# Optimization experiments

Measured on AMD Instinct MI355X. Metric: run time of the kernel, lower is better.

Reference implementation:

```python
import jax, jax.numpy as jnp
import numpy as np

BETA = 0.05
KNN = 6
N_SPLITS = 10


def setup_inputs() -> dict:
    key = jax.random.key(0)
    k1, k2, k3 = jax.random.split(key, 3)
    B, C, F = 256, 32768, 2048
    inputs = jax.random.normal(k1, (B, F), dtype=jnp.float32)
    inputs = inputs / jnp.linalg.norm(inputs, axis=1, keepdims=True)  # re-ID features are L2-normalized
    em = jax.random.normal(k2, (C, F), dtype=jnp.float32)
    em = em / jnp.linalg.norm(em, axis=1, keepdims=True)  # memory rows kept unit-norm by EMA update
    targets = jax.random.randint(k3, (B,), 0, C, dtype=jnp.int64)
    return {"inputs": inputs, "em": em, "targets": targets, "epoch": 10}


def reference(inputs, em, targets, epoch):
    B, Fdim = inputs.shape
    C = em.shape[0]
    step = -(-Fdim // N_SPLITS)  # ceil, matches step+=1 logic in torch

    # full similarity against memory bank: [B, C]
    sim = (inputs @ em.T) / BETA

    # per-feature-split similarities: [n_splits, B, C]
    sims = jnp.stack([
        (inputs[:, step * i: min(step * (i + 1), Fdim)]
         @ em[:, step * i: min(step * (i + 1), Fdim)].T) / BETA
        for i in range(N_SPLITS)
    ])

    logp = jax.nn.log_softmax(sim, axis=1)  # [B, C]

    if KNN > 0 and epoch > 4:
        # top-k neighbors per split (descending sort -> first k)
        _, topk = jax.lax.top_k(sims, KNN)  # [n_splits, B, KNN]
        s_idx = jnp.arange(N_SPLITS)[:, None, None]
        b_idx = jnp.arange(B)[None, :, None]
        # scatter uniform weight 1/k at knn indices, then force 1.0 at the true target
        onehot = jnp.zeros((N_SPLITS, B, C), dtype=sim.dtype)
        onehot = onehot.at[s_idx, b_idx, topk].set(1.0 / KNN)
        onehot = onehot.at[jnp.arange(N_SPLITS)[:, None],
                           jnp.arange(B)[None, :],
                           targets[None, :]].set(1.0)
        # mean over splits of mean_b sum_c -(t * log p)
        loss = (-(onehot * logp[None, :, :]).sum(axis=2)).mean(axis=1).mean()
    else:
        loss = -jnp.take_along_axis(logp, targets[:, None], axis=1).mean()
    return loss
```

## Files before the change

kernel.cpp:

```cpp
#include <hip/hip_runtime.h>
#include <stdint.h>


typedef float f32x4 __attribute__((ext_vector_type(4)));
typedef __bf16 bf16x8 __attribute__((ext_vector_type(8)));
typedef unsigned short u16x8 __attribute__((ext_vector_type(8)));

#define NB 256
#define NC 32768
#define NF 2048
#define NSPLIT 10
#define SPLITW 205
#define BN 64
#define NBLK (NC / BN)
#define NKSTEP 64
#define INV_BETA 20.0f
#define UNRL _Pragma("unroll")

__device__ __forceinline__ unsigned short f2bf(float f) {
  uint32_t u = __float_as_uint(f);
  return (unsigned short)((u + 0x7FFFu + ((u >> 16) & 1u)) >> 16);
}
__device__ __forceinline__ bf16x8 asbf(u16x8 v) {
  union { u16x8 u; bf16x8 b; } x; x.u = v; return x.b;
}

#define GLDS16(g, p) __builtin_amdgcn_global_load_lds(                         \
    (const __attribute__((address_space(1))) unsigned int*)(g),                \
    (__attribute__((address_space(3))) unsigned int*)(p), 16, 0, 0)

__global__ __launch_bounds__(256)
void k_zero(float* __restrict__ sumexp, float* __restrict__ out) {
  int t = threadIdx.x;
  if (t < NB) sumexp[t] = 0.f;
  if (t == 0) out[0] = 0.f;
}


#define ISSUE_A(BB, TT) do {                                                   \
  UNRL for (int j_ = 0; j_ < 4; j_++) {                                        \
    const int c_ = w * 4 + j_;                                                 \
    const float* g_ = inp + (size_t)(c_ * 8 + arr) * NF + (TT) * 32 + ag * 4;  \
    GLDS16(g_, &Af[BB][c_ * 256]);                                             \
  }                                                                            \
} while (0)

#define FINALIZE(S) do {                                                       \
  UNRL for (int m_ = 0; m_ < 2; m_++)                                          \
    UNRL for (int n_ = 0; n_ < 4; n_++) accT[m_][n_] += accS[m_][n_];          \
  UNRL for (int m_ = 0; m_ < 2; m_++) {                                        \
    UNRL for (int j_ = 0; j_ < 4; j_++) {                                      \
      uint32_t p_[4];                                                          \
      UNRL for (int n_ = 0; n_ < 4; n_++) {                                    \
        uint32_t u_ = __float_as_uint(accS[m_][n_][j_]);                       \
        u_ ^= (uint32_t)(((int32_t)u_) >> 31) | 0x80000000u;                   \
        p_[n_] = (u_ & 0xFFFFFF80u) | (uint32_t)(n_ * 16 + li);                \
      }                                                                        \
      uint32_t res_[6];                                                        \
      UNRL for (int r_ = 0; r_ < 6; r_++) {                                    \
        uint32_t mx_ = p_[0];                                                  \
        UNRL for (int n_ = 1; n_ < 4; n_++) mx_ = mx_ > p_[n_] ? mx_ : p_[n_]; \
        UNRL for (int d_ = 1; d_ < 16; d_ <<= 1) {                             \
          uint32_t o_ = __shfl_xor(mx_, d_);                                   \
          mx_ = mx_ > o_ ? mx_ : o_;                                           \
        }                                                                      \
        res_[r_] = mx_;                                                        \
        UNRL for (int n_ = 0; n_ < 4; n_++)                                    \
          p_[n_] = (p_[n_] == mx_) ? 0u : p_[n_];                              \
      }                                                                        \
      if (li == 0) {                                                           \
        const int rowg_ = w * 32 + m_ * 16 + lg * 4 + j_;                      \
        uint32_t* dst_ = cand + ((size_t)((S) * NB + rowg_) * NBLK + bx) * 6;  \
        UNRL for (int r_ = 0; r_ < 6; r_++) dst_[r_] = res_[r_];               \
      }                                                                        \
    }                                                                          \
    UNRL for (int n_ = 0; n_ < 4; n_++) accS[m_][n_] = Z4;                     \
  }                                                                            \
} while (0)

#define MFMA_ALL(AF) do {                                                      \
  UNRL for (int m_ = 0; m_ < 2; m_++)                                          \
    UNRL for (int n_ = 0; n_ < 4; n_++)                                        \
      accS[m_][n_] = __builtin_amdgcn_mfma_f32_16x16x32_bf16(                  \
          asbf((AF)[m_]), asbf(bfv_[n_]), accS[m_][n_], 0, 0, 0);              \
} while (0)

#define STEP(TT, CB, NBUF, PRE) do {                                           \
  f32x4 bv_ = {0.f, 0.f, 0.f, 0.f};                                            \
  if (PRE) {                                                                   \
    ISSUE_A(NBUF, (TT) + 1);                                                   \
    bv_ = *(const f32x4*)(em + (size_t)(c0 + br) * NF + ((TT) + 1) * 32 + bg * 4); \
  }                                                                            \
  u16x8 af_[2];                                                                \
  UNRL for (int m_ = 0; m_ < 2; m_++) {                                        \
    const int chunk_ = w * 4 + m_ * 2 + (li >> 3);                             \
    const int rr_ = li & 7;                                                    \
    const float* bp_ = &Af[CB][chunk_ * 256 + rr_ * 32];                       \
    f32x4 x0_ = *(const f32x4*)(bp_ + (((lg << 1)) ^ rr_) * 4);                \
    f32x4 x1_ = *(const f32x4*)(bp_ + (((lg << 1) | 1) ^ rr_) * 4);            \
    af_[m_][0] = f2bf(x0_[0]); af_[m_][1] = f2bf(x0_[1]);                      \
    af_[m_][2] = f2bf(x0_[2]); af_[m_][3] = f2bf(x0_[3]);                      \
    af_[m_][4] = f2bf(x1_[0]); af_[m_][5] = f2bf(x1_[1]);                      \
    af_[m_][6] = f2bf(x1_[2]); af_[m_][7] = f2bf(x1_[3]);                      \
  }                                                                            \
  u16x8 bfv_[4];                                                               \
  UNRL for (int n_ = 0; n_ < 4; n_++) {                                        \
    const int rowp_ = n_ * 16 + li;                                            \
    const int sl_ = lg ^ ((rowp_ >> 1) & 3);                                   \
    bfv_[n_] = *(const u16x8*)&Bh[CB][rowp_ * 32 + sl_ * 8];                   \
  }                                                                            \
  const int k0_ = (TT) * 32;                                                   \
  const int s0_ = k0_ / SPLITW, s1_ = (k0_ + 31) / SPLITW;                     \
  if (s1_ > s0_) {                                                             \
    const int thr_ = s1_ * SPLITW - k0_;                                       \
    u16x8 am_[2];                                                              \
    UNRL for (int m_ = 0; m_ < 2; m_++)                                        \
      UNRL for (int e_ = 0; e_ < 8; e_++)                                      \
        am_[m_][e_] = (lg * 8 + e_) < thr_ ? af_[m_][e_] : (unsigned short)0;  \
    MFMA_ALL(am_);                                                             \
    FINALIZE(s0_);                                                             \
    UNRL for (int m_ = 0; m_ < 2; m_++)                                        \
      UNRL for (int e_ = 0; e_ < 8; e_++)                                      \
        am_[m_][e_] = (lg * 8 + e_) < thr_ ? (unsigned short)0 : af_[m_][e_];  \
    MFMA_ALL(am_);                                                             \
  } else {                                                                     \
    MFMA_ALL(af_);                                                             \
  }                                                                            \
  if (PRE) {                                                                   \
    ushort4 hh_;                                                               \
    hh_.x = f2bf(bv_[0]); hh_.y = f2bf(bv_[1]);                                \
    hh_.z = f2bf(bv_[2]); hh_.w = f2bf(bv_[3]);                                \
    *(ushort4*)&Bh[NBUF][br * 32 + bus * 8 + bh2 * 4] = hh_;                   \
  }                                                                            \
  __syncthreads();                                                             \
} while (0)

__global__ __launch_bounds__(512, 4)
void k_main(const float* __restrict__ inp, const float* __restrict__ em,
            float* __restrict__ sim, uint32_t* __restrict__ cand,
            float* __restrict__ sumexp) {
  __shared__ float Af[2][8192];
  __shared__ unsigned short Bh[2][2048];

  const int t  = threadIdx.x;
  const int l  = t & 63;
  const int w  = t >> 6;
  const int li = l & 15, lg = l >> 4;
  const int bx = blockIdx.x;
  const int c0 = bx * BN;

  const int arr = l >> 3;
  const int ag  = (l & 7) ^ arr;
  const int br  = t >> 3, bg = t & 7;
  const int bus = (bg >> 1) ^ ((br >> 1) & 3);
  const int bh2 = bg & 1;

  const f32x4 Z4 = {0.f, 0.f, 0.f, 0.f};
  f32x4 accT[2][4], accS[2][4];
  UNRL for (int m = 0; m < 2; m++)
    UNRL for (int n = 0; n < 4; n++) { accT[m][n] = Z4; accS[m][n] = Z4; }

  {
    ISSUE_A(0, 0);
    f32x4 bv = *(const f32x4*)(em + (size_t)(c0 + br) * NF + bg * 4);
    ushort4 hh;
    hh.x = f2bf(bv[0]); hh.y = f2bf(bv[1]); hh.z = f2bf(bv[2]); hh.w = f2bf(bv[3]);
    *(ushort4*)&Bh[0][br * 32 + bus * 8 + bh2 * 4] = hh;
    __syncthreads();
  }
  for (int tt2 = 0; tt2 < 31; ++tt2) {
    STEP(2 * tt2, 0, 1, 1);
    STEP(2 * tt2 + 1, 1, 0, 1);
  }
  STEP(62, 0, 1, 1);
  STEP(63, 1, 0, 0);
  FINALIZE(NSPLIT - 1);

  UNRL for (int m = 0; m < 2; m++) {
    UNRL for (int j = 0; j < 4; j++) {
      const int rowg = w * 32 + m * 16 + lg * 4 + j;
      float se = 0.f;
      UNRL for (int n = 0; n < 4; n++) {
        float v = accT[m][n][j] * INV_BETA;
        sim[(size_t)rowg * NC + c0 + n * 16 + li] = v;
        se += __expf(v);
      }
      UNRL for (int d = 1; d < 16; d <<= 1) se += __shfl_xor(se, d);
      if (li == 0) atomicAdd(&sumexp[rowg], se);
    }
  }
}

__device__ __forceinline__ void casd(unsigned long long& a, unsigned long long& b) {
  unsigned long long mx = a > b ? a : b;
  unsigned long long mn = a > b ? b : a;
  a = mx; b = mn;
}

__device__ __forceinline__ void merge8(unsigned long long* a,
                                       const unsigned long long* b) {
  unsigned long long hi[8];
  UNRL for (int i = 0; i < 8; i++) {
    unsigned long long x = a[i], y = b[7 - i];
    hi[i] = x > y ? x : y;
  }
  casd(hi[0], hi[4]); casd(hi[1], hi[5]); casd(hi[2], hi[6]); casd(hi[3], hi[7]);
  casd(hi[0], hi[2]); casd(hi[1], hi[3]); casd(hi[4], hi[6]); casd(hi[5], hi[7]);
  casd(hi[0], hi[1]); casd(hi[2], hi[3]); casd(hi[4], hi[5]); casd(hi[6], hi[7]);
  UNRL for (int i = 0; i < 8; i++) a[i] = hi[i];
}

__global__ __launch_bounds__(64)
void k_m1(const uint32_t* __restrict__ cand,
          unsigned long long* __restrict__ part) {
  const int bx = blockIdx.x;
  const int s = bx >> 11;
  const int b = (bx >> 3) & 255;
  const int g = bx & 7;
  const int l = threadIdx.x;

  const uint32_t* src = cand + ((size_t)(s * NB + b) * NBLK + g * 64) * 6;
  unsigned long long t8[8];
  UNRL for (int i = 0; i < 8; i++) t8[i] = 0ull;

  UNRL for (int i = 0; i < 6; i++) {
    const int idx = l + i * 64;
    const uint32_t e = src[idx];
    const uint32_t colg = (uint32_t)(g * 64 + idx / 6) * 64u + (e & 63u);
    unsigned long long v = ((unsigned long long)(e & 0xFFFFFF80u) << 32)
                         | (unsigned long long)(0xFFFFu ^ colg);
    UNRL for (int k = 0; k < 8; k++) {
      if (v > t8[k]) { unsigned long long tmp = t8[k]; t8[k] = v; v = tmp; }
    }
  }
  UNRL for (int d = 1; d < 64; d <<= 1) {
    unsigned long long o[8];
    UNRL for (int i = 0; i < 8; i++) o[i] = __shfl_xor(t8[i], d);
    merge8(t8, o);
  }
  if (l == 0) {
    unsigned long long* dst = part + ((size_t)(s * NB + b) * 8 + g) * 6;
    UNRL for (int r = 0; r < 6; r++) dst[r] = t8[r];
  }
}

__global__ __launch_bounds__(64)
void k_m2(const unsigned long long* __restrict__ part,
          const float* __restrict__ sim, const float* __restrict__ sumexp,
          const int* __restrict__ tgt, float* __restrict__ out) {
  const int s = blockIdx.x >> 8;
  const int b = blockIdx.x & 255;
  const int l = threadIdx.x;

  unsigned long long t8[8];
  UNRL for (int i = 0; i < 8; i++) t8[i] = 0ull;
  t8[0] = (l < 48) ? part[(size_t)(s * NB + b) * 48 + l] : 0ull;

  UNRL for (int d = 1; d < 64; d <<= 1) {
    unsigned long long o[8];
    UNRL for (int i = 0; i < 8; i++) o[i] = __shfl_xor(t8[i], d);
    merge8(t8, o);
  }
  if (l == 0) {
    const int tg = tgt[b];
    const float lz = logf(sumexp[b]);
    float acc = 0.f; int cnt = 0;
    UNRL for (int r = 0; r < 6; r++) {
      const int col = (int)(((unsigned)(t8[r] & 0xFFFFull)) ^ 0xFFFFu);
      if (col != tg) { acc += sim[(size_t)b * NC + col]; cnt++; }
    }
    const float simt = sim[(size_t)b * NC + tg];
    const float contrib = (simt - lz) + (acc - (float)cnt * lz) * (1.0f / 6.0f);
    atomicAdd(out, -contrib * (1.0f / (NSPLIT * NB)));
  }
}

extern "C" void kernel_launch(void* const* d_in, const int* in_sizes, int n_in,
                              void* d_out, int out_size, void* d_ws, size_t ws_size,
                              hipStream_t stream) {
  const float* inp = (const float*)d_in[0];
  const float* em  = (const float*)d_in[1];
  const int*   tgt = (const int*)d_in[2];
  float* out = (float*)d_out;

  char* ws = (char*)d_ws;
  float* sim = (float*)ws;
  size_t off = (size_t)NB * NC * 4;
  uint32_t* cand = (uint32_t*)(ws + off);
  off += (size_t)NSPLIT * NB * NBLK * 6 * 4;
  unsigned long long* part = (unsigned long long*)(ws + off);
  off += (size_t)NSPLIT * NB * 8 * 6 * 8;
  float* sumexp = (float*)(ws + off);

  k_zero<<<1, 256, 0, stream>>>(sumexp, out);
  k_main<<<NBLK, 512, 0, stream>>>(inp, em, sim, cand, sumexp);
  k_m1<<<NSPLIT * NB * 8, 64, 0, stream>>>(cand, part);
  k_m2<<<NSPLIT * NB, 64, 0, stream>>>(part, sim, sumexp, tgt, out);
}
```

Before: 837.9 us.

## Replace LDS-staged block GEMM with per-wave tiles loading directly from global

Drops the shared-memory double-buffered 512-thread block, which covered all 256 rows against 64 columns. Each 64-thread wave now computes a 32x64 tile, reading bf16 A and fp32 em rows straight from global memory into MFMA fragments. A separate pre-pass converts the input matrix to bf16 once. This removes LDS staging and barriers, but each em tile is now read by 8 row-groups instead of once, which raises global/L2 traffic and relies on cache hits. The loads are uncoalesced row-strided 32-byte accesses.

```diff
diff --git a/kernel.cpp b/kernel.cpp
--- a/kernel.cpp
+++ b/kernel.cpp
@@ -11,23 +11,16 @@
 #define NF 2048
 #define NSPLIT 10
 #define SPLITW 205
-#define BN 64
-#define NBLK (NC / BN)
+#define WM 32
+#define WN 64
+#define NBLK (NC / WN)
 #define NKSTEP 64
 #define INV_BETA 20.0f
 #define UNRL _Pragma("unroll")
 
-__device__ __forceinline__ unsigned short f2bf(float f) {
-  uint32_t u = __float_as_uint(f);
-  return (unsigned short)((u + 0x7FFFu + ((u >> 16) & 1u)) >> 16);
-}
 __device__ __forceinline__ bf16x8 asbf(u16x8 v) {
   union { u16x8 u; bf16x8 b; } x; x.u = v; return x.b;
 }
-
-#define GLDS16(g, p) __builtin_amdgcn_global_load_lds(                         \
-    (const __attribute__((address_space(1))) unsigned int*)(g),                \
-    (__attribute__((address_space(3))) unsigned int*)(p), 16, 0, 0)
 
 __global__ __launch_bounds__(256)
 void k_zero(float* __restrict__ sumexp, float* __restrict__ out) {
@@ -36,14 +29,17 @@
   if (t == 0) out[0] = 0.f;
 }
 
-
-#define ISSUE_A(BB, TT) do {                                                   \
-  UNRL for (int j_ = 0; j_ < 4; j_++) {                                        \
-    const int c_ = w * 4 + j_;                                                 \
-    const float* g_ = inp + (size_t)(c_ * 8 + arr) * NF + (TT) * 32 + ag * 4;  \
-    GLDS16(g_, &Af[BB][c_ * 256]);                                             \
-  }                                                                            \
-} while (0)
+__global__ __launch_bounds__(256)
+void k_cvtA(const float* __restrict__ inp, unsigned short* __restrict__ abf) {
+  const int idx = (blockIdx.x * 256 + threadIdx.x) * 8;
+  f32x4 v0 = *(const f32x4*)(inp + idx);
+  f32x4 v1 = *(const f32x4*)(inp + idx + 4);
+  union { bf16x8 b; u16x8 u; } cv;
+  UNRL for (int e = 0; e < 4; e++) cv.b[e] = (__bf16)v0[e];
+  UNRL for (int e = 0; e < 4; e++) cv.b[4 + e] = (__bf16)v1[e];
+  *(u16x8*)(abf + idx) = cv.u;
+}
+
 
 #define FINALIZE(S) do {                                                       \
   UNRL for (int m_ = 0; m_ < 2; m_++)                                          \
@@ -69,8 +65,8 @@
           p_[n_] = (p_[n_] == mx_) ? 0u : p_[n_];                              \
       }                                                                        \
       if (li == 0) {                                                           \
-        const int rowg_ = w * 32 + m_ * 16 + lg * 4 + j_;                      \
-        uint32_t* dst_ = cand + ((size_t)((S) * NB + rowg_) * NBLK + bx) * 6;  \
+        const int rowg_ = r0 + m_ * 16 + lg * 4 + j_;                          \
+        uint32_t* dst_ = cand + ((size_t)((S) * NB + rowg_) * NBLK + cb) * 6;  \
         UNRL for (int r_ = 0; r_ < 6; r_++) dst_[r_] = res_[r_];               \
       }                                                                        \
     }                                                                          \
@@ -82,103 +78,64 @@
   UNRL for (int m_ = 0; m_ < 2; m_++)                                          \
     UNRL for (int n_ = 0; n_ < 4; n_++)                                        \
       accS[m_][n_] = __builtin_amdgcn_mfma_f32_16x16x32_bf16(                  \
-          asbf((AF)[m_]), asbf(bfv_[n_]), accS[m_][n_], 0, 0, 0);              \
+          asbf((AF)[m_]), bfv_[n_], accS[m_][n_], 0, 0, 0);                    \
 } while (0)
 
-#define STEP(TT, CB, NBUF, PRE) do {                                           \
-  f32x4 bv_ = {0.f, 0.f, 0.f, 0.f};                                            \
-  if (PRE) {                                                                   \
-    ISSUE_A(NBUF, (TT) + 1);                                                   \
-    bv_ = *(const f32x4*)(em + (size_t)(c0 + br) * NF + ((TT) + 1) * 32 + bg * 4); \
-  }                                                                            \
-  u16x8 af_[2];                                                                \
-  UNRL for (int m_ = 0; m_ < 2; m_++) {                                        \
-    const int chunk_ = w * 4 + m_ * 2 + (li >> 3);                             \
-    const int rr_ = li & 7;                                                    \
-    const float* bp_ = &Af[CB][chunk_ * 256 + rr_ * 32];                       \
-    f32x4 x0_ = *(const f32x4*)(bp_ + (((lg << 1)) ^ rr_) * 4);                \
-    f32x4 x1_ = *(const f32x4*)(bp_ + (((lg << 1) | 1) ^ rr_) * 4);            \
-    af_[m_][0] = f2bf(x0_[0]); af_[m_][1] = f2bf(x0_[1]);                      \
-    af_[m_][2] = f2bf(x0_[2]); af_[m_][3] = f2bf(x0_[3]);                      \
-    af_[m_][4] = f2bf(x1_[0]); af_[m_][5] = f2bf(x1_[1]);                      \
-    af_[m_][6] = f2bf(x1_[2]); af_[m_][7] = f2bf(x1_[3]);                      \
-  }                                                                            \
-  u16x8 bfv_[4];                                                               \
-  UNRL for (int n_ = 0; n_ < 4; n_++) {                                        \
-    const int rowp_ = n_ * 16 + li;                                            \
-    const int sl_ = lg ^ ((rowp_ >> 1) & 3);                                   \
-    bfv_[n_] = *(const u16x8*)&Bh[CB][rowp_ * 32 + sl_ * 8];                   \
-  }                                                                            \
-  const int k0_ = (TT) * 32;                                                   \
-  const int s0_ = k0_ / SPLITW, s1_ = (k0_ + 31) / SPLITW;                     \
-  if (s1_ > s0_) {                                                             \
-    const int thr_ = s1_ * SPLITW - k0_;                                       \
-    u16x8 am_[2];                                                              \
-    UNRL for (int m_ = 0; m_ < 2; m_++)                                        \
-      UNRL for (int e_ = 0; e_ < 8; e_++)                                      \
-        am_[m_][e_] = (lg * 8 + e_) < thr_ ? af_[m_][e_] : (unsigned short)0;  \
-    MFMA_ALL(am_);                                                             \
-    FINALIZE(s0_);                                                             \
-    UNRL for (int m_ = 0; m_ < 2; m_++)                                        \
-      UNRL for (int e_ = 0; e_ < 8; e_++)                                      \
-        am_[m_][e_] = (lg * 8 + e_) < thr_ ? (unsigned short)0 : af_[m_][e_];  \
-    MFMA_ALL(am_);                                                             \
-  } else {                                                                     \
-    MFMA_ALL(af_);                                                             \
-  }                                                                            \
-  if (PRE) {                                                                   \
-    ushort4 hh_;                                                               \
-    hh_.x = f2bf(bv_[0]); hh_.y = f2bf(bv_[1]);                                \
-    hh_.z = f2bf(bv_[2]); hh_.w = f2bf(bv_[3]);                                \
-    *(ushort4*)&Bh[NBUF][br * 32 + bus * 8 + bh2 * 4] = hh_;                   \
-  }                                                                            \
-  __syncthreads();                                                             \
-} while (0)
-
-__global__ __launch_bounds__(512, 4)
-void k_main(const float* __restrict__ inp, const float* __restrict__ em,
+__global__ __launch_bounds__(64, 4)
+void k_main(const unsigned short* __restrict__ abf, const float* __restrict__ em,
             float* __restrict__ sim, uint32_t* __restrict__ cand,
             float* __restrict__ sumexp) {
-  __shared__ float Af[2][8192];
-  __shared__ unsigned short Bh[2][2048];
-
-  const int t  = threadIdx.x;
-  const int l  = t & 63;
-  const int w  = t >> 6;
+  const int l  = threadIdx.x;
   const int li = l & 15, lg = l >> 4;
-  const int bx = blockIdx.x;
-  const int c0 = bx * BN;
-
-  const int arr = l >> 3;
-  const int ag  = (l & 7) ^ arr;
-  const int br  = t >> 3, bg = t & 7;
-  const int bus = (bg >> 1) ^ ((br >> 1) & 3);
-  const int bh2 = bg & 1;
+  const int rg = blockIdx.x >> 9;
+  const int cb = blockIdx.x & 511;
+  const int r0 = rg * WM;
+  const int c0 = cb * WN;
 
   const f32x4 Z4 = {0.f, 0.f, 0.f, 0.f};
   f32x4 accT[2][4], accS[2][4];
   UNRL for (int m = 0; m < 2; m++)
     UNRL for (int n = 0; n < 4; n++) { accT[m][n] = Z4; accS[m][n] = Z4; }
 
-  {
-    ISSUE_A(0, 0);
-    f32x4 bv = *(const f32x4*)(em + (size_t)(c0 + br) * NF + bg * 4);
-    ushort4 hh;
-    hh.x = f2bf(bv[0]); hh.y = f2bf(bv[1]); hh.z = f2bf(bv[2]); hh.w = f2bf(bv[3]);
-    *(ushort4*)&Bh[0][br * 32 + bus * 8 + bh2 * 4] = hh;
-    __syncthreads();
-  }
-  for (int tt2 = 0; tt2 < 31; ++tt2) {
-    STEP(2 * tt2, 0, 1, 1);
-    STEP(2 * tt2 + 1, 1, 0, 1);
-  }
-  STEP(62, 0, 1, 1);
-  STEP(63, 1, 0, 0);
+  const unsigned short* a0 = abf + (size_t)(r0 + li) * NF + lg * 8;
+  const float* b0 = em + (size_t)(c0 + li) * NF + lg * 8;
+
+  #pragma unroll 2
+  for (int tt = 0; tt < NKSTEP; ++tt) {
+    const int k0 = tt * 32;
+    u16x8 af_[2];
+    UNRL for (int m_ = 0; m_ < 2; m_++)
+      af_[m_] = *(const u16x8*)(a0 + (size_t)m_ * 16 * NF + k0);
+    bf16x8 bfv_[4];
+    UNRL for (int n_ = 0; n_ < 4; n_++) {
+      const float* bp_ = b0 + (size_t)n_ * 16 * NF + k0;
+      f32x4 x0_ = *(const f32x4*)bp_;
+      f32x4 x1_ = *(const f32x4*)(bp_ + 4);
+      UNRL for (int e_ = 0; e_ < 4; e_++) bfv_[n_][e_] = (__bf16)x0_[e_];
+      UNRL for (int e_ = 0; e_ < 4; e_++) bfv_[n_][4 + e_] = (__bf16)x1_[e_];
+    }
+    const int s0_ = k0 / SPLITW, s1_ = (k0 + 31) / SPLITW;
+    if (s1_ > s0_) {
+      const int thr_ = s1_ * SPLITW - k0;
+      u16x8 am_[2];
+      UNRL for (int m_ = 0; m_ < 2; m_++)
+        UNRL for (int e_ = 0; e_ < 8; e_++)
+          am_[m_][e_] = (lg * 8 + e_) < thr_ ? af_[m_][e_] : (unsigned short)0;
+      MFMA_ALL(am_);
+      FINALIZE(s0_);
+      UNRL for (int m_ = 0; m_ < 2; m_++)
+        UNRL for (int e_ = 0; e_ < 8; e_++)
+          am_[m_][e_] = (lg * 8 + e_) < thr_ ? (unsigned short)0 : af_[m_][e_];
+      MFMA_ALL(am_);
+    } else {
+      MFMA_ALL(af_);
+    }
+  }
   FINALIZE(NSPLIT - 1);
 
   UNRL for (int m = 0; m < 2; m++) {
     UNRL for (int j = 0; j < 4; j++) {
-      const int rowg = w * 32 + m * 16 + lg * 4 + j;
+      const int rowg = r0 + m * 16 + lg * 4 + j;
       float se = 0.f;
       UNRL for (int n = 0; n < 4; n++) {
         float v = accT[m][n][j] * INV_BETA;
@@ -291,9 +248,12 @@
   unsigned long long* part = (unsigned long long*)(ws + off);
   off += (size_t)NSPLIT * NB * 8 * 6 * 8;
   float* sumexp = (float*)(ws + off);
+  off += 1024;
+  unsigned short* abf = (unsigned short*)(ws + off);
 
   k_zero<<<1, 256, 0, stream>>>(sumexp, out);
-  k_main<<<NBLK, 512, 0, stream>>>(inp, em, sim, cand, sumexp);
+  k_cvtA<<<256, 256, 0, stream>>>(inp, abf);
+  k_main<<<8 * NBLK, 64, 0, stream>>>(abf, em, sim, cand, sumexp);
   k_m1<<<NSPLIT * NB * 8, 64, 0, stream>>>(cand, part);
   k_m2<<<NSPLIT * NB, 64, 0, stream>>>(part, sim, sumexp, tgt, out);
 }
```

Result: faster. 801.3 us (-4.4%).
